# Kernel optimization log

Hardware: AMD Instinct MI355X
Metric: run time of the kernel (lower is better)

## Reference

```python
import jax, jax.numpy as jnp
from jax import lax
import numpy as np

SCALE = 3.0
TOPK = 16  # eigvec[:, -16:] in the original module
BN_EPS = 1e-5
DN = ('NCHW', 'OIHW', 'NCHW')


def setup_inputs() -> dict:
    key = jax.random.key(0)
    ks = jax.random.split(key, 8)
    B, C, H, W = 16, 256, 64, 64
    x = jax.random.normal(ks[0], (B, C, H, W), dtype=jnp.float32)
    conv1_w = jax.random.normal(ks[1], (C, C, 1, 1), dtype=jnp.float32) * (1.0 / np.sqrt(C))
    conv1_b = jax.random.normal(ks[2], (C,), dtype=jnp.float32) * 0.01
    conv2_w = jax.random.normal(ks[3], (C, C, 3, 3), dtype=jnp.float32) * (1.0 / np.sqrt(9 * C))
    bn_gamma = jnp.ones((C,), dtype=jnp.float32)
    bn_beta = jnp.zeros((C,), dtype=jnp.float32)
    bn_mean = jax.random.normal(ks[4], (C,), dtype=jnp.float32) * 0.1
    bn_var = jax.random.uniform(ks[5], (C,), dtype=jnp.float32, minval=0.5, maxval=1.5)
    return {"x": x, "conv1_w": conv1_w, "conv1_b": conv1_b, "conv2_w": conv2_w,
            "bn_gamma": bn_gamma, "bn_beta": bn_beta, "bn_mean": bn_mean, "bn_var": bn_var}


def reference(x, conv1_w, conv1_b, conv2_w, bn_gamma, bn_beta, bn_mean, bn_var):
    B, C, H, W = x.shape
    # conv1: 1x1 conv with bias
    gx = lax.conv_general_dilated(x, conv1_w, (1, 1), 'SAME', dimension_numbers=DN)
    gx = gx + conv1_b[None, :, None, None]
    # center over spatial positions: [B, C, N]
    g = gx.reshape(B, C, H * W)
    g = g - jnp.mean(g, axis=-1, keepdims=True)
    # per-batch covariance, divided by batch size (faithful to original gx.shape[0])
    cmat = jnp.einsum('bcn,bdn->bcd', g, g) / B  # [B, C, C]
    # batched symmetric eigendecomposition (ascending eigenvalues, like torch.symeig)
    _, vecs = jnp.linalg.eigh(cmat)              # vecs: [B, C, C]
    w = jnp.swapaxes(vecs[..., -TOPK:], -1, -2)  # top-16 eigvecs, [B, 16, C]
    # project onto eigvec subspace, softmax over the 16 components (dim=1)
    z = jax.nn.softmax(jnp.einsum('bkc,bcn->bkn', w, g) * SCALE, axis=1)  # [B, 16, N]
    y = jnp.einsum('bkc,bkn->bcn', w, z).reshape(B, C, H, W)
    # conv2: 3x3 conv (no bias) + BatchNorm (eval mode with running stats)
    att = lax.conv_general_dilated(y, conv2_w, (1, 1), 'SAME', dimension_numbers=DN)
    inv = bn_gamma * lax.rsqrt(bn_var + BN_EPS)
    att = att * inv[None, :, None, None] + (bn_beta - bn_mean * inv)[None, :, None, None]
    return x + att
```

## Files before the change

### kernel.cpp

```cpp
#include <hip/hip_runtime.h>
#include <hip/hip_bf16.h>
#include <math.h>


typedef __hip_bfloat16 bf16;

#define NB 16
#define NC 256
#define NSP 4096
#define LAPACK_EPS32 5.9604644775390625e-08

__device__ __forceinline__ float b2f(bf16 v){ return __bfloat162float(v); }
__device__ __forceinline__ double safelog(double x){
  double a = fabs(x);
  if (!(a > 0.0) || !isfinite(a)) a = 1e-300;
  return log(a);
}

__global__ __launch_bounds__(256) void k_detect(const unsigned short* __restrict__ xr,
                                                int* __restrict__ flags){
  __shared__ int red[256];
  int tid = threadIdx.x;
  int cnt = 0;
  for (int i = tid; i < 4096; i += 256){
    unsigned int u = xr[i];
    unsigned int e = (u >> 7) & 0xFF;
    if (e >= 134) ++cnt;
  }
  red[tid] = cnt; __syncthreads();
  for (int o=128;o>0;o>>=1){ if(tid<o) red[tid]+=red[tid+o]; __syncthreads(); }
  if (tid==0) flags[0] = (red[0] > 50) ? 1 : 0;
}

__global__ __launch_bounds__(256) void k_conv1(const void* __restrict__ xv_,
                                               const void* __restrict__ w1v,
                                               const int* __restrict__ flags,
                                               float* __restrict__ g){
  __shared__ float ws[16][256];
  int nt = blockIdx.x, ct = blockIdx.y, b = blockIdx.z;
  int tid = threadIdx.x;
  int c0 = ct*16;
  int isf = flags[0];
  if (isf){
    const float* w1 = (const float*)w1v;
    for (int i = tid; i < 16*256; i += 256)
      ws[i>>8][i&255] = w1[(size_t)(c0 + (i>>8))*256 + (i&255)];
  } else {
    const bf16* w1 = (const bf16*)w1v;
    for (int i = tid; i < 16*256; i += 256)
      ws[i>>8][i&255] = b2f(w1[(size_t)(c0 + (i>>8))*256 + (i&255)]);
  }
  __syncthreads();
  int n = nt*256 + tid;
  float acc[16];
  #pragma unroll
  for (int i=0;i<16;++i) acc[i]=0.f;
  if (isf){
    const float* xp = (const float*)xv_ + (size_t)b*NC*NSP + n;
    for (int d=0; d<256; ++d){
      float xv = xp[(size_t)d*NSP];
      #pragma unroll
      for (int i=0;i<16;++i) acc[i] = fmaf(ws[i][d], xv, acc[i]);
    }
  } else {
    const bf16* xp = (const bf16*)xv_ + (size_t)b*NC*NSP + n;
    for (int d=0; d<256; ++d){
      float xv = b2f(xp[(size_t)d*NSP]);
      #pragma unroll
      for (int i=0;i<16;++i) acc[i] = fmaf(ws[i][d], xv, acc[i]);
    }
  }
  float* gp = g + ((size_t)b*NC + c0)*NSP + n;
  #pragma unroll
  for (int i=0;i<16;++i) gp[(size_t)i*NSP] = acc[i];
}

__global__ __launch_bounds__(256) void k_center(float* __restrict__ g){
  int bc = blockIdx.x;
  float* p = g + (size_t)bc*NSP;
  int tid = threadIdx.x;
  __shared__ float red[256];
  float s = 0.f;
  for (int i=tid;i<NSP;i+=256) s += p[i];
  red[tid]=s; __syncthreads();
  for (int o=128;o>0;o>>=1){ if(tid<o) red[tid]+=red[tid+o]; __syncthreads(); }
  float mean = red[0] * (1.0f/4096.0f);
  for (int i=tid;i<NSP;i+=256) p[i] -= mean;
}

__global__ __launch_bounds__(256) void k_cmat(const float* __restrict__ g,
                                              float* __restrict__ A){
  __shared__ float t1[32][65];
  __shared__ float t2[32][65];
  int bx = blockIdx.x, by = blockIdx.y, b = blockIdx.z;
  int tid = threadIdx.x;
  int tx = tid & 31, ty = tid >> 5;
  const float* gb = g + (size_t)b*NC*NSP;
  float acc[4] = {0.f,0.f,0.f,0.f};
  for (int ch=0; ch<64; ++ch){
    int n0 = ch*64;
    for (int idx=tid; idx<2048; idx+=256){
      int r = idx>>6, cc = idx&63;
      t1[r][cc] = gb[(size_t)(by*32 + r)*NSP + n0 + cc];
      t2[r][cc] = gb[(size_t)(bx*32 + r)*NSP + n0 + cc];
    }
    __syncthreads();
    for (int kk=0; kk<64; ++kk){
      float v2 = t2[tx][kk];
      #pragma unroll
      for (int jj=0;jj<4;++jj) acc[jj] = fmaf(t1[ty+8*jj][kk], v2, acc[jj]);
    }
    __syncthreads();
  }
  #pragma unroll
  for (int jj=0;jj<4;++jj){
    int row = by*32 + ty + 8*jj, col = bx*32 + tx;
    A[((size_t)b*NC + row)*NC + col] = acc[jj]*(1.0f/16.0f);
  }
}

__global__ __launch_bounds__(256,1) void k_sytd2(float* __restrict__ Ag,
                                                 float* __restrict__ e_g,
                                                 float* __restrict__ tau_g,
                                                 float* __restrict__ d_g){
  int b = blockIdx.x, tid = threadIdx.x;
  float* A = Ag + (size_t)b*65536;
  __shared__ float v[256], wv[256], red[256];
  __shared__ float sc[2];
  for (int i=0;i<255;++i){
    float s=0.f;
    for (int r=i+2+tid; r<256; r+=256){ float a=A[(size_t)i*256+r]; s+=a*a; }
    red[tid]=s; __syncthreads();
    for(int o=128;o>0;o>>=1){ if(tid<o) red[tid]+=red[tid+o]; __syncthreads(); }
    if (tid==0){
      float xnorm2 = red[0];
      float alpha = A[(size_t)i*256+(i+1)];
      float tau=0.f, scale=0.f, beta=alpha;
      if (xnorm2 > 0.f){
        float r_ = sqrtf(alpha*alpha + xnorm2);
        beta = (alpha >= 0.f) ? -r_ : r_;
        tau = (beta - alpha)/beta;
        scale = 1.0f/(alpha - beta);
      }
      e_g[b*256+i] = beta; tau_g[b*256+i] = tau;
      sc[0]=tau; sc[1]=scale;
    }
    __syncthreads();
    float tau = sc[0], scale = sc[1];
    if (tau != 0.f){
      for (int r=i+1+tid; r<256; r+=256){
        float val = (r==i+1)?1.0f : A[(size_t)i*256+r]*scale;
        A[(size_t)i*256+r] = val;  v[r] = val;
      }
      __syncthreads();
      for (int r=i+1+tid; r<256; r+=256){
        const float* Ar = A + r;
        float acc=0.f;
        int c2 = i+1;
        for (; c2+16<=256; c2+=16){
          float av[16], vv[16];
          #pragma unroll
          for (int u=0;u<16;++u) av[u] = Ar[(size_t)(c2+u)*256];
          #pragma unroll
          for (int u=0;u<16;++u) vv[u] = v[c2+u];
          #pragma unroll
          for (int u=0;u<16;++u) acc = fmaf(av[u], vv[u], acc);
        }
        for (; c2<256; ++c2) acc = fmaf(Ar[(size_t)c2*256], v[c2], acc);
        wv[r] = tau*acc;
      }
      __syncthreads();
      float sd=0.f;
      for (int r=i+1+tid;r<256;r+=256) sd += v[r]*wv[r];
      red[tid]=sd; __syncthreads();
      for(int o=128;o>0;o>>=1){ if(tid<o) red[tid]+=red[tid+o]; __syncthreads(); }
      float a2 = -0.5f*tau*red[0];
      for (int r=i+1+tid;r<256;r+=256) wv[r] += a2*v[r];
      __syncthreads();
      int r = i+1+tid;
      if (r < 256){
        float vr=v[r], wr=wv[r];
        float* Arw = A + r;
        int c2 = i+1;
        for (; c2+16<=256; c2+=16){
          float av[16], wvv[16], vvv[16];
          #pragma unroll
          for (int u=0;u<16;++u) av[u]  = Arw[(size_t)(c2+u)*256];
          #pragma unroll
          for (int u=0;u<16;++u) wvv[u] = wv[c2+u];
          #pragma unroll
          for (int u=0;u<16;++u) vvv[u] = v[c2+u];
          #pragma unroll
          for (int u=0;u<16;++u) av[u] -= vr*wvv[u] + wr*vvv[u];
          #pragma unroll
          for (int u=0;u<16;++u) Arw[(size_t)(c2+u)*256] = av[u];
        }
        for (; c2<256; ++c2)
          Arw[(size_t)c2*256] -= vr*wv[c2] + wr*v[c2];
      }
      __syncthreads();
    }
    __syncthreads();
  }
  for (int r=tid;r<256;r+=256) d_g[b*256+r] = A[(size_t)r*256+r];
}

__global__ __launch_bounds__(256) void k_leaf(const float* __restrict__ d_g,
                                              const float* __restrict__ e_g,
                                              float* __restrict__ Qg,
                                              double* __restrict__ Dw_g,
                                              double* __restrict__ emod_g){
  int b = blockIdx.x, tid = threadIdx.x;
  float* Q = Qg + (size_t)b*65536;
  double* Dw = Dw_g + (size_t)b*256;
  __shared__ double As[16*257];
  __shared__ float  Vt[16*257];
  __shared__ double dms[256];
  __shared__ double emod[256];
  __shared__ float redf[256];

  float dv = d_g[b*256+tid];
  float ev = (tid<255)? e_g[b*256+tid] : 0.f;
  redf[tid] = fmaxf(fabsf(dv), fabsf(ev)); __syncthreads();
  for(int o=128;o>0;o>>=1){ if(tid<o) redf[tid]=fmaxf(redf[tid],redf[tid+o]); __syncthreads(); }
  double sigma = (double)redf[0];
  if (!(sigma > 0.0)) sigma = 1.0;
  double dmod = (double)dv;
  if ((tid & 15)==15 && tid<255) dmod -= fabs((double)e_g[b*256+tid]);
  if ((tid & 15)==0  && tid>0)   dmod -= fabs((double)e_g[b*256+tid-1]);
  dmod /= sigma;
  double em = (tid<255)? ((double)ev)/sigma : 0.0;
  dms[tid] = dmod;  emod[tid] = em;
  emod_g[b*256+tid] = em;
  __syncthreads();

  int l16 = tid & ~15, j = tid & 15;
  for (int r=0;r<16;++r){
    double av = 0.0;
    if (r==j)        av = dms[l16+j];
    else if (r==j-1) av = emod[l16+j-1];
    else if (r==j+1) av = emod[l16+j];
    As[r*257+tid] = av;
    Vt[r*257+tid] = (r==j)? 1.f : 0.f;
  }
  __syncthreads();

  for (int sweep=0; sweep<14; ++sweep){
    for (int p=0;p<15;++p){
      for (int q=p+1;q<16;++q){
        double app = As[p*257 + l16+p];
        double aqq = As[q*257 + l16+q];
        double apq = As[p*257 + l16+q];
        bool rot = (fabs(apq) > 1e-18);
        double c, s;
        if (rot){
          double theta = (aqq - app)/(2.0*apq);
          double t = 1.0/(fabs(theta)+sqrt(1.0+theta*theta));
          if (theta < 0.0) t = -t;
          c = 1.0/sqrt(1.0+t*t); s = t*c;
        } else { c = 1.0; s = 0.0; }
        double apj = As[p*257 + tid];
        double aqj = As[q*257 + tid];
        double npj = c*apj - s*aqj;
        double nqj = s*apj + c*aqj;
        if (rot && j==p){ npj = c*c*app - 2.0*c*s*apq + s*s*aqq; nqj = 0.0; }
        if (rot && j==q){ npj = 0.0; nqj = s*s*app + 2.0*c*s*apq + c*c*aqq; }
        As[p*257 + tid] = npj;
        As[q*257 + tid] = nqj;
        As[j*257 + l16+p] = npj;
        As[j*257 + l16+q] = nqj;
        float vp = Vt[p*257 + tid], vq = Vt[q*257 + tid];
        Vt[p*257 + tid] = (float)(c*(double)vp - s*(double)vq);
        Vt[q*257 + tid] = (float)(s*(double)vp + c*(double)vq);
      }
    }
  }
  __syncthreads();
  double myval = As[j*257 + l16+j];
  int rank = 0;
  for (int k=0;k<16;++k){
    double vk = As[k*257 + l16+k];
    if (vk < myval || (vk==myval && k<j)) ++rank;
  }
  Dw[l16+rank] = myval;
  for (int r=0;r<16;++r)
    Q[(size_t)(l16+r)*256 + (l16+rank)] = Vt[j*257 + l16+r];
}

struct DCMerge {
  double z_[256], dsv[256], ds2[256], zs2[256];
  double dl_[256], zl_[256], taus[256], ztil[256], normk[256], evo[256];
  double rotcs[256][2];
  int    cs2[256], colx[256], non_[256], defl_[256], anch[256], osrc[256], otyp[256];
  int    roti[256][2];
};

__global__ __launch_bounds__(256) void k_msolve(int lev,
                                                const double* __restrict__ emod_g,
                                                float* __restrict__ Qsrc,
                                                double* __restrict__ Dw_g,
                                                double* __restrict__ Sdl,
                                                double* __restrict__ Sztil,
                                                double* __restrict__ Staus,
                                                double* __restrict__ Snk,
                                                int* __restrict__ Scolx,
                                                int* __restrict__ Sanch,
                                                int* __restrict__ Sotyp,
                                                int* __restrict__ Sosrc,
                                                int* __restrict__ SK){
  int mrg = blockIdx.x, b = blockIdx.y, tid = threadIdx.x;
  float* Q  = Qsrc + (size_t)b*65536;
  double* Dw = Dw_g + (size_t)b*256;
  int slot = b*8 + mrg;
  __shared__ DCMerge mg;
  __shared__ int bci[4];

  int ssz = 16<<lev, nm = ssz<<1;
  int base = mrg*nm;
  double rho0 = emod_g[b*256 + base+ssz-1];
  if (tid < nm){
    float zf = (tid < ssz) ? Q[(size_t)(base+ssz-1)*256 + base + tid]
                           : Q[(size_t)(base+ssz)*256   + base + tid];
    double zz = (double)zf;
    if (rho0 < 0.0 && tid >= ssz) zz = -zz;
    mg.z_[tid] = zz * 0.70710678118654752440;
    mg.dsv[tid] = Dw[base+tid];
  }
  __syncthreads();
  double rho = fabs(2.0*rho0);
  if (tid==0){
    int i1=0, i2=ssz, o=0;
    while (i1<ssz || i2<nm){
      bool take1;
      if (i1>=ssz) take1=false; else if (i2>=nm) take1=true;
      else take1 = (mg.dsv[i1] <= mg.dsv[i2]);
      int src = take1? i1++ : i2++;
      mg.ds2[o]=mg.dsv[src]; mg.zs2[o]=mg.z_[src]; mg.cs2[o]=src; ++o;
    }
  }
  __syncthreads();
  mg.taus[tid] = (tid<nm)? fabs(mg.zs2[tid]) : 0.0; __syncthreads();
  for(int o2=128;o2>0;o2>>=1){ if(tid<o2) mg.taus[tid]=fmax(mg.taus[tid],mg.taus[tid+o2]); __syncthreads(); }
  double zmax = mg.taus[0]; __syncthreads();
  mg.taus[tid] = (tid<nm)? fabs(mg.ds2[tid]) : 0.0; __syncthreads();
  for(int o2=128;o2>0;o2>>=1){ if(tid<o2) mg.taus[tid]=fmax(mg.taus[tid],mg.taus[tid+o2]); __syncthreads(); }
  double dmax = mg.taus[0]; __syncthreads();
  double tol = 8.0*LAPACK_EPS32*fmax(dmax, zmax);
  if (tid==0){
    int K=0, nd=0, nrot=0, pj=-1;
    for (int j=0;j<nm;++j){
      if (rho*fabs(mg.zs2[j]) <= tol){ mg.defl_[nd++]=j; continue; }
      if (pj>=0){
        double sg=mg.zs2[pj], cg=mg.zs2[j];
        double tg=mg.ds2[j]-mg.ds2[pj];
        double taug=sqrt(cg*cg+sg*sg);
        double cn, sn;
        if (taug > 0.0){ cn=cg/taug; sn=-sg/taug; } else { cn=1.0; sn=0.0; }
        if (fabs(tg*cn*sn) <= tol){
          mg.zs2[j]=taug; mg.zs2[pj]=0.0;
          mg.roti[nrot][0]=mg.cs2[pj]; mg.roti[nrot][1]=mg.cs2[j];
          mg.rotcs[nrot][0]=cn; mg.rotcs[nrot][1]=sn; ++nrot;
          double t2 = mg.ds2[pj]*cn*cn + mg.ds2[j]*sn*sn;
          mg.ds2[j] = mg.ds2[pj]*sn*sn + mg.ds2[j]*cn*cn;
          mg.ds2[pj] = t2;
          mg.defl_[nd++]=pj;
          pj=j;
        } else { mg.non_[K++]=pj; pj=j; }
      } else pj=j;
    }
    if (pj>=0) mg.non_[K++]=pj;
    bci[0]=K; bci[1]=nd; bci[2]=nrot;
  }
  __syncthreads();
  int K=bci[0], nd=bci[1], nrot=bci[2];
  for (int r2=0;r2<nrot;++r2){
    int ca = base + mg.roti[r2][0], cb2 = base + mg.roti[r2][1];
    double cn = mg.rotcs[r2][0], sn = mg.rotcs[r2][1];
    if (tid < nm){
      int row = base+tid;
      float xv = Q[(size_t)row*256+ca], yv = Q[(size_t)row*256+cb2];
      Q[(size_t)row*256+ca]  = (float)(cn*(double)xv + sn*(double)yv);
      Q[(size_t)row*256+cb2] = (float)(cn*(double)yv - sn*(double)xv);
    }
    __syncthreads();
  }
  if (tid<K){
    mg.dl_[tid]=mg.ds2[mg.non_[tid]];
    mg.zl_[tid]=mg.zs2[mg.non_[tid]];
    mg.colx[tid]=mg.cs2[mg.non_[tid]];
  }
  __syncthreads();
  mg.taus[tid] = (tid<K)? mg.zl_[tid]*mg.zl_[tid] : 0.0; __syncthreads();
  for(int o2=128;o2>0;o2>>=1){ if(tid<o2) mg.taus[tid]+=mg.taus[tid+o2]; __syncthreads(); }
  double zsum2 = mg.taus[0]; __syncthreads();
  if (tid<K){
    int j=tid;
    double left=mg.dl_[j];
    double right=(j<K-1)? mg.dl_[j+1] : (mg.dl_[K-1] + rho*zsum2);
    double mid=0.5*(left+right);
    double fm=1.0;
    for (int i3=0;i3<K;++i3){
      double del=mg.dl_[i3]-mid;
      fm += rho*mg.zl_[i3]*mg.zl_[i3]/del;
    }
    int a; double lo, hi;
    if (j==K-1){
      a=K-1;
      if (fm<=0.0){ lo=mid-left; hi=right-left; } else { lo=0.0; hi=mid-left; }
    } else if (fm<=0.0){ a=j+1; lo=mid-mg.dl_[j+1]; hi=0.0; }
    else { a=j; lo=0.0; hi=mid-left; }
    double da2=mg.dl_[a];
    double t;
    if (hi > lo){
      t=0.5*(lo+hi);
    } else {
      t = (a==j)? 1e-300 : -1e-300;
      lo = fmin(lo, t); hi = fmax(hi, t);
    }
    for (int it=0; it<100; ++it){
      double gg=1.0, dg=0.0;
      for (int i3=0;i3<K;++i3){
        double del=(mg.dl_[i3]-da2)-t;
        double q=mg.zl_[i3]/del;
        gg += rho*mg.zl_[i3]*q;
        dg += rho*q*q;
      }
      if (gg<0.0) lo=t; else hi=t;
      double tn = t - gg/dg;
      if (!isfinite(tn) || !(tn>lo && tn<hi)) tn=0.5*(lo+hi);
      if (tn == 0.0) tn = (t!=0.0)? t*0.5 : ((a==j)?1e-300:-1e-300);
      double dstep=fabs(tn-t);
      t=tn;
      if (dstep <= 1e-15*(fabs(t)+1e-30)) break;
      if ((hi-lo) <= 1e-15*(fabs(da2)+fabs(t)+1e-30)) break;
    }
    if (t == 0.0 || !isfinite(t)) t = (a==j)? 1e-300 : -1e-300;
    mg.taus[j]=t; mg.anch[j]=a;
  }
  __syncthreads();
  if (tid<K){
    int i3=tid; double acc=0.0; double di=mg.dl_[i3];
    for (int j=0;j<K;++j){
      double lmd = (mg.dl_[mg.anch[j]] - di) + mg.taus[j];
      acc += safelog(lmd);
      if (j!=i3) acc -= safelog(mg.dl_[j]-di);
    }
    double mag = exp(0.5*acc);
    if (!isfinite(mag)) mag = 0.0;
    mg.ztil[i3] = (mg.zl_[i3] >= 0.0)? mag : -mag;
  }
  __syncthreads();
  if (tid<K){
    int j=tid; double da2=mg.dl_[mg.anch[j]]; double tj=mg.taus[j];
    double nr=0.0;
    for (int i3=0;i3<K;++i3){
      double del=(mg.dl_[i3]-da2)-tj;
      if (del == 0.0) del = (tj>=0.0)? -1e-300 : 1e-300;
      double sv=mg.ztil[i3]/del;
      nr += sv*sv;
    }
    if (!(nr > 0.0) || !isfinite(nr)) nr = 1.0;
    mg.normk[j]=sqrt(nr);
  }
  __syncthreads();
  if (tid==0){
    for (int a2=1;a2<nd;++a2){
      int key=mg.defl_[a2]; double kv=mg.ds2[key]; int b2=a2-1;
      while (b2>=0 && mg.ds2[mg.defl_[b2]] > kv){ mg.defl_[b2+1]=mg.defl_[b2]; --b2; }
      mg.defl_[b2+1]=key;
    }
    int i1=0,i2=0,o=0;
    while (i1<K || i2<nd){
      double v1 = (i1<K)? (mg.dl_[mg.anch[i1]]+mg.taus[i1]) : 0.0;
      double v2 = (i2<nd)? mg.ds2[mg.defl_[i2]] : 0.0;
      bool take1;
      if (i1>=K) take1=false; else if (i2>=nd) take1=true; else take1 = (v1 <= v2);
      if (take1){ mg.otyp[o]=0; mg.osrc[o]=i1; mg.evo[o]=v1; ++i1; }
      else { mg.otyp[o]=1; mg.osrc[o]=mg.cs2[mg.defl_[i2]]; mg.evo[o]=v2; ++i2; }
      ++o;
    }
  }
  __syncthreads();
  if (tid<nm) Dw[base+tid]=mg.evo[tid];
  size_t so = (size_t)slot*256;
  if (tid<K){
    Sdl[so+tid]=mg.dl_[tid]; Sztil[so+tid]=mg.ztil[tid];
    Staus[so+tid]=mg.taus[tid]; Snk[so+tid]=mg.normk[tid];
    Scolx[so+tid]=mg.colx[tid]; Sanch[so+tid]=mg.anch[tid];
  }
  if (tid<nm){ Sotyp[so+tid]=mg.otyp[tid]; Sosrc[so+tid]=mg.osrc[tid]; }
  if (tid==0) SK[slot]=K;
}

__global__ __launch_bounds__(256) void k_mvec(int lev,
                                              const float* __restrict__ Qsrc_g,
                                              float* __restrict__ Qdst_g,
                                              const double* __restrict__ Sdl,
                                              const double* __restrict__ Sztil,
                                              const double* __restrict__ Staus,
                                              const double* __restrict__ Snk,
                                              const int* __restrict__ Scolx,
                                              const int* __restrict__ Sanch,
                                              const int* __restrict__ Sotyp,
                                              const int* __restrict__ Sosrc,
                                              const int* __restrict__ SK){
  int t = blockIdx.x, mrg = blockIdx.y, b = blockIdx.z, tid = threadIdx.x;
  const float* Q = Qsrc_g + (size_t)b*65536;
  float* Qd = Qdst_g + (size_t)b*65536;
  int slot = b*8 + mrg;
  size_t so = (size_t)slot*256;
  int ssz = 16<<lev, nm = ssz<<1;
  int base = mrg*nm;
  int p0 = t*16;
  int K = SK[slot];

  __shared__ float svf[256*16];
  __shared__ double cda[16], ctj[16];
  __shared__ float cnk[16];
  __shared__ int ctyp[16], csrc[16];

  if (tid < 16){
    int p = p0 + tid;
    int typ = Sotyp[so+p], src = Sosrc[so+p];
    ctyp[tid]=typ; csrc[tid]=src;
    if (typ==0){
      int j = src;
      cda[tid] = Sdl[so + Sanch[so+j] - 0 + 0];
    }
  }
  __syncthreads();
  if (tid < 16){
    int p = p0 + tid;
    if (ctyp[tid]==0){
      int j = csrc[tid];
      int a = Sanch[so+j];
      cda[tid] = Sdl[so+a];
      ctj[tid] = Staus[so+j];
      cnk[tid] = (float)Snk[so+j];
    } else { cda[tid]=0.0; ctj[tid]=1.0; cnk[tid]=1.f; }
  }
  __syncthreads();
  for (int idx = tid; idx < K*16; idx += 256){
    int i3 = idx >> 4, c = idx & 15;
    float sv = 0.f;
    if (ctyp[c]==0){
      double del = (Sdl[so+i3] - cda[c]) - ctj[c];
      if (del == 0.0) del = (ctj[c]>=0.0)? -1e-300 : 1e-300;
      sv = (float)( Sztil[so+i3]/del / (double)cnk[c] );
      if (!isfinite(sv)) sv = 0.f;
    }
    svf[i3*16 + c] = sv;
  }
  __syncthreads();

  if (tid < nm){
    int row = base + tid;
    const float* Qr = Q + (size_t)row*256 + base;
    float acc[16];
    #pragma unroll
    for (int c=0;c<16;++c) acc[c]=0.f;
    for (int i3=0;i3<K;++i3){
      float qv = Qr[Scolx[so+i3]];
      #pragma unroll
      for (int c=0;c<16;++c) acc[c] = fmaf(qv, svf[i3*16+c], acc[c]);
    }
    #pragma unroll
    for (int c=0;c<16;++c){
      float v = acc[c];
      if (ctyp[c]==1) v = Qr[csrc[c]];
      if (!isfinite(v)) v = 0.f;
      Qd[(size_t)row*256 + base + p0 + c] = v;
    }
  }
}

__global__ __launch_bounds__(256,1) void k_backtf(const float* __restrict__ Ag,
                                                  const float* __restrict__ tau_g,
                                                  const float* __restrict__ Qg,
                                                  float* __restrict__ w16g){
  int b=blockIdx.x, tid=threadIdx.x;
  const float* A=Ag+(size_t)b*65536;
  const float* Q=Qg+(size_t)b*65536;
  __shared__ float U[256][17];
  __shared__ float pd[16][17];
  __shared__ float dk[16];
  int k=tid&15, rg=tid>>4;
  for (int r=rg;r<256;r+=16) U[r][k]=Q[(size_t)r*256+240+k];
  __syncthreads();
  for (int i=254;i>=0;--i){
    float tau=tau_g[b*256+i];
    if (tau!=0.f){
      int r0 = i+1+rg;
      float ar[16];
      #pragma unroll
      for (int u=0;u<16;++u){
        int r = r0 + u*16;
        ar[u] = (r<256)? A[(size_t)i*256+r] : 0.f;
      }
      float uv[16];
      #pragma unroll
      for (int u=0;u<16;++u){
        int r = r0 + u*16;
        uv[u] = (r<256)? U[r][k] : 0.f;
      }
      float s=0.f;
      #pragma unroll
      for (int u=0;u<16;++u){
        int r = r0 + u*16;
        if (r<256) s += ar[u]*uv[u];
      }
      pd[rg][k]=s;
      __syncthreads();
      if (tid<16){
        float acc=0.f;
        #pragma unroll
        for (int gg=0; gg<16; ++gg) acc+=pd[gg][tid];
        dk[tid]=tau*acc;
      }
      __syncthreads();
      float dkk = dk[k];
      #pragma unroll
      for (int u=0;u<16;++u){
        int r = r0 + u*16;
        if (r<256) U[r][k] -= dkk*ar[u];
      }
      __syncthreads();
    }
  }
  for (int c2=rg;c2<256;c2+=16){
    float uv = U[c2][k];
    if (!isfinite(uv)) uv = 0.f;
    w16g[((size_t)b*16+k)*256+c2]=uv;
  }
}

__global__ __launch_bounds__(256) void k_score(const float* __restrict__ g,
                                               const float* __restrict__ w16,
                                               float* __restrict__ z){
  __shared__ float ws[16][256];
  int nt=blockIdx.x, b=blockIdx.y, tid=threadIdx.x;
  for (int i=tid;i<4096;i+=256) ws[i>>8][i&255]=w16[(size_t)b*4096+i];
  __syncthreads();
  int n=nt*256+tid;
  const float* gp=g+(size_t)b*NC*NSP+n;
  float acc[16];
  #pragma unroll
  for(int k2=0;k2<16;++k2) acc[k2]=0.f;
  for (int c2=0;c2<256;++c2){
    float gv=gp[(size_t)c2*NSP];
    #pragma unroll
    for (int k2=0;k2<16;++k2) acc[k2]=fmaf(ws[k2][c2],gv,acc[k2]);
  }
  float mx=-1e30f;
  #pragma unroll
  for(int k2=0;k2<16;++k2){ acc[k2]*=3.0f; mx=fmaxf(mx,acc[k2]); }
  float sum=0.f;
  #pragma unroll
  for(int k2=0;k2<16;++k2){ acc[k2]=expf(acc[k2]-mx); sum+=acc[k2]; }
  float inv=1.0f/sum;
  float* zp=z+(size_t)b*16*NSP+n;
  #pragma unroll
  for(int k2=0;k2<16;++k2) zp[(size_t)k2*NSP]=acc[k2]*inv;
}

__global__ __launch_bounds__(256) void k_y(const float* __restrict__ z,
                                           const float* __restrict__ w16,
                                           float* __restrict__ y){
  __shared__ float ws[16][256];
  int nt=blockIdx.x, b=blockIdx.y, tid=threadIdx.x;
  for (int i=tid;i<4096;i+=256) ws[i>>8][i&255]=w16[(size_t)b*4096+i];
  __syncthreads();
  int n=nt*256+tid;
  const float* zp=z+(size_t)b*16*NSP+n;
  float zr[16];
  #pragma unroll
  for(int k2=0;k2<16;++k2) zr[k2]=zp[(size_t)k2*NSP];
  float* yp=y+(size_t)b*NC*NSP+n;
  for (int c2=0;c2<256;++c2){
    float acc=0.f;
    #pragma unroll
    for (int k2=0;k2<16;++k2) acc=fmaf(ws[k2][c2],zr[k2],acc);
    yp[(size_t)c2*NSP]=acc;
  }
}

__global__ __launch_bounds__(256) void k_conv2(const float* __restrict__ y,
                                               const void* __restrict__ w2v,
                                               const void* __restrict__ xv_,
                                               const void* __restrict__ gmv,
                                               const void* __restrict__ btv,
                                               const void* __restrict__ muv,
                                               const void* __restrict__ vrv,
                                               const int* __restrict__ flags,
                                               void* __restrict__ outv){
  __shared__ float yt[8][6][66];
  __shared__ float wt[16][8][9];
  int ht=blockIdx.x, ct=blockIdx.y, b=blockIdx.z, tid=threadIdx.x;
  int hl=tid>>6, wl=tid&63;
  int h=ht*4+hl;
  int c0=ct*16;
  int isf = flags[0];
  float acc[16];
  #pragma unroll
  for(int i=0;i<16;++i) acc[i]=0.f;
  const float* yb = y + (size_t)b*NC*NSP;
  for (int d0=0; d0<256; d0+=8){
    for (int idx=tid; idx<8*6*64; idx+=256){
      int dd=idx/384; int rem=idx-dd*384; int rr=rem>>6; int cc2=rem&63;
      int hg=ht*4-1+rr;
      float v = (hg>=0 && hg<64)? yb[(size_t)(d0+dd)*NSP + hg*64 + cc2] : 0.f;
      yt[dd][rr][cc2+1]=v;
    }
    if (tid<48){ int dd=tid/6, rr=tid-dd*6; yt[dd][rr][0]=0.f; yt[dd][rr][65]=0.f; }
    if (isf){
      const float* w2 = (const float*)w2v;
      for (int idx=tid; idx<16*8*9; idx+=256){
        int cc=idx/72; int rem=idx-cc*72; int dd=rem/9; int kk=rem-dd*9;
        wt[cc][dd][kk]=w2[ ((size_t)(c0+cc)*256 + d0+dd)*9 + kk ];
      }
    } else {
      const bf16* w2 = (const bf16*)w2v;
      for (int idx=tid; idx<16*8*9; idx+=256){
        int cc=idx/72; int rem=idx-cc*72; int dd=rem/9; int kk=rem-dd*9;
        wt[cc][dd][kk]=b2f(w2[ ((size_t)(c0+cc)*256 + d0+dd)*9 + kk ]);
      }
    }
    __syncthreads();
    for (int cc=0; cc<16; ++cc){
      float a=acc[cc];
      #pragma unroll
      for (int dd=0; dd<8; ++dd){
        const float* wp=wt[cc][dd];
        a = fmaf(wp[0], yt[dd][hl+0][wl+0], a);
        a = fmaf(wp[1], yt[dd][hl+0][wl+1], a);
        a = fmaf(wp[2], yt[dd][hl+0][wl+2], a);
        a = fmaf(wp[3], yt[dd][hl+1][wl+0], a);
        a = fmaf(wp[4], yt[dd][hl+1][wl+1], a);
        a = fmaf(wp[5], yt[dd][hl+1][wl+2], a);
        a = fmaf(wp[6], yt[dd][hl+2][wl+0], a);
        a = fmaf(wp[7], yt[dd][hl+2][wl+1], a);
        a = fmaf(wp[8], yt[dd][hl+2][wl+2], a);
      }
      acc[cc]=a;
    }
    __syncthreads();
  }
  size_t nidx=(size_t)h*64+wl;
  for (int cc=0;cc<16;++cc){
    int c=c0+cc;
    float gmf, btf, muf, vrf, xvv;
    size_t oi = ((size_t)b*NC+c)*NSP + nidx;
    if (isf){
      gmf=((const float*)gmv)[c]; btf=((const float*)btv)[c];
      muf=((const float*)muv)[c]; vrf=((const float*)vrv)[c];
      xvv=((const float*)xv_)[oi];
    } else {
      gmf=b2f(((const bf16*)gmv)[c]); btf=b2f(((const bf16*)btv)[c]);
      muf=b2f(((const bf16*)muv)[c]); vrf=b2f(((const bf16*)vrv)[c]);
      xvv=b2f(((const bf16*)xv_)[oi]);
    }
    float inv = gmf * rsqrtf(vrf + 1e-5f);
    float shift = btf - muf*inv;
    float val = xvv + acc[cc]*inv + shift;
    if (isf) ((float*)outv)[oi] = val;
    else     ((bf16*)outv)[oi] = __float2bfloat16(val);
  }
}

extern "C" void kernel_launch(void* const* d_in, const int* in_sizes, int n_in,
                              void* d_out, int out_size, void* d_ws, size_t ws_size,
                              hipStream_t stream) {
  const void* x   = d_in[0];
  const void* w1  = d_in[1];
  const void* w2  = d_in[3];
  const void* gmm = d_in[4];
  const void* bet = d_in[5];
  const void* mu  = d_in[6];
  const void* var = d_in[7];

  float* g    = (float*)d_ws;
  float* A    = g   + (size_t)NB*NC*NSP;
  float* Qa   = A   + (size_t)NB*NC*NC;
  float* Qb   = Qa  + (size_t)NB*NC*NC;
  float* w16  = Qb  + (size_t)NB*NC*NC;
  float* zb   = w16 + (size_t)NB*16*NC;
  float* e_g  = zb  + (size_t)NB*16*NSP;
  float* tau_g= e_g + (size_t)NB*NC;
  float* d_g  = tau_g + (size_t)NB*NC;
  double* Dw  = (double*)(d_g + (size_t)NB*NC);
  double* emod_g = Dw + (size_t)NB*NC;
  double* Sdl   = emod_g + (size_t)NB*NC;
  double* Sztil = Sdl   + (size_t)128*256;
  double* Staus = Sztil + (size_t)128*256;
  double* Snk   = Staus + (size_t)128*256;
  int* Scolx = (int*)(Snk + (size_t)128*256);
  int* Sanch = Scolx + (size_t)128*256;
  int* Sotyp = Sanch + (size_t)128*256;
  int* Sosrc = Sotyp + (size_t)128*256;
  int* SK    = Sosrc + (size_t)128*256;
  int* flags = SK + 256;
  size_t needed = (size_t)((char*)(flags + 16) - (char*)d_ws);
  if (ws_size < needed) return;

  hipMemsetAsync(Qa, 0, (size_t)NB*NC*NC*2*sizeof(float), stream);
  k_detect<<<dim3(1),256,0,stream>>>((const unsigned short*)x, flags);
  k_conv1 <<<dim3(16,16,16),256,0,stream>>>(x, w1, flags, g);
  k_center<<<dim3(NB*NC),256,0,stream>>>(g);
  k_cmat  <<<dim3(8,8,16),256,0,stream>>>(g, A);
  k_sytd2 <<<dim3(16),256,0,stream>>>(A, e_g, tau_g, d_g);
  k_leaf  <<<dim3(16),256,0,stream>>>(d_g, e_g, Qa, Dw, emod_g);
  k_msolve<<<dim3(8,16),256,0,stream>>>(0, emod_g, Qa, Dw, Sdl,Sztil,Staus,Snk,Scolx,Sanch,Sotyp,Sosrc,SK);
  k_mvec  <<<dim3(2,8,16),256,0,stream>>>(0, Qa, Qb, Sdl,Sztil,Staus,Snk,Scolx,Sanch,Sotyp,Sosrc,SK);
  k_msolve<<<dim3(4,16),256,0,stream>>>(1, emod_g, Qb, Dw, Sdl,Sztil,Staus,Snk,Scolx,Sanch,Sotyp,Sosrc,SK);
  k_mvec  <<<dim3(4,4,16),256,0,stream>>>(1, Qb, Qa, Sdl,Sztil,Staus,Snk,Scolx,Sanch,Sotyp,Sosrc,SK);
  k_msolve<<<dim3(2,16),256,0,stream>>>(2, emod_g, Qa, Dw, Sdl,Sztil,Staus,Snk,Scolx,Sanch,Sotyp,Sosrc,SK);
  k_mvec  <<<dim3(8,2,16),256,0,stream>>>(2, Qa, Qb, Sdl,Sztil,Staus,Snk,Scolx,Sanch,Sotyp,Sosrc,SK);
  k_msolve<<<dim3(1,16),256,0,stream>>>(3, emod_g, Qb, Dw, Sdl,Sztil,Staus,Snk,Scolx,Sanch,Sotyp,Sosrc,SK);
  k_mvec  <<<dim3(16,1,16),256,0,stream>>>(3, Qb, Qa, Sdl,Sztil,Staus,Snk,Scolx,Sanch,Sotyp,Sosrc,SK);
  k_backtf<<<dim3(16),256,0,stream>>>(A, tau_g, Qa, w16);
  k_score <<<dim3(16,16),256,0,stream>>>(g, w16, zb);
  k_y     <<<dim3(16,16),256,0,stream>>>(zb, w16, g);
  k_conv2 <<<dim3(16,16,16),256,0,stream>>>(g, w2, x, gmm, bet, mu, var, flags, d_out);
}
```

Baseline: 8.107 ms.

## Move trailing tridiagonalization submatrix into shared memory and double-buffer global loads

The Householder tridiagonalization kernel is split into two phases. The first 80 reflections still run on the global-memory matrix, now with 32-wide double-buffered loads in the symv and rank-2 update loops. The remaining 176x176 trailing block is then copied into LDS (about 124 KB) and the later steps run entirely out of shared memory. The block reduction is also replaced with a shuffle-based version, and every thread now computes tau and scale redundantly, which removes a barrier and the shared scalar broadcast. The large LDS allocation caps occupancy at one block per CU, and the 64-float register buffers add register pressure.

```diff
diff --git a/kernel.cpp b/kernel.cpp
--- a/kernel.cpp
+++ b/kernel.cpp
@@ -9,12 +9,29 @@
 #define NC 256
 #define NSP 4096
 #define LAPACK_EPS32 5.9604644775390625e-08
+
+#define PHB_I0 80
+#define PHB_M  176
 
 __device__ __forceinline__ float b2f(bf16 v){ return __bfloat162float(v); }
 __device__ __forceinline__ double safelog(double x){
   double a = fabs(x);
   if (!(a > 0.0) || !isfinite(a)) a = 1e-300;
   return log(a);
+}
+
+__device__ __forceinline__ float blk_reduce_sum(float s, float* red, int tid){
+  red[tid] = s; __syncthreads();
+  if (tid < 128) red[tid] += red[tid+128];
+  __syncthreads();
+  if (tid < 64){
+    float x = red[tid] + red[tid+64];
+    #pragma unroll
+    for (int o = 32; o > 0; o >>= 1) x += __shfl_down(x, o);
+    if (tid == 0) red[0] = x;
+  }
+  __syncthreads();
+  return red[0];
 }
 
 __global__ __launch_bounds__(256) void k_detect(const unsigned short* __restrict__ xr,
@@ -125,28 +142,22 @@
                                                  float* __restrict__ d_g){
   int b = blockIdx.x, tid = threadIdx.x;
   float* A = Ag + (size_t)b*65536;
+  __shared__ float Asub[PHB_M*PHB_M];
   __shared__ float v[256], wv[256], red[256];
-  __shared__ float sc[2];
-  for (int i=0;i<255;++i){
+
+  for (int i=0;i<PHB_I0;++i){
+    float alpha = A[(size_t)i*256+(i+1)];
     float s=0.f;
     for (int r=i+2+tid; r<256; r+=256){ float a=A[(size_t)i*256+r]; s+=a*a; }
-    red[tid]=s; __syncthreads();
-    for(int o=128;o>0;o>>=1){ if(tid<o) red[tid]+=red[tid+o]; __syncthreads(); }
-    if (tid==0){
-      float xnorm2 = red[0];
-      float alpha = A[(size_t)i*256+(i+1)];
-      float tau=0.f, scale=0.f, beta=alpha;
-      if (xnorm2 > 0.f){
-        float r_ = sqrtf(alpha*alpha + xnorm2);
-        beta = (alpha >= 0.f) ? -r_ : r_;
-        tau = (beta - alpha)/beta;
-        scale = 1.0f/(alpha - beta);
-      }
-      e_g[b*256+i] = beta; tau_g[b*256+i] = tau;
-      sc[0]=tau; sc[1]=scale;
-    }
-    __syncthreads();
-    float tau = sc[0], scale = sc[1];
+    float xnorm2 = blk_reduce_sum(s, red, tid);
+    float tau=0.f, scale=0.f, beta=alpha;
+    if (xnorm2 > 0.f){
+      float r_ = sqrtf(alpha*alpha + xnorm2);
+      beta = (alpha >= 0.f) ? -r_ : r_;
+      tau = (beta - alpha)/beta;
+      scale = 1.0f/(alpha - beta);
+    }
+    if (tid==0){ e_g[b*256+i] = beta; tau_g[b*256+i] = tau; }
     if (tau != 0.f){
       for (int r=i+1+tid; r<256; r+=256){
         float val = (r==i+1)?1.0f : A[(size_t)i*256+r]*scale;
@@ -156,53 +167,171 @@
       for (int r=i+1+tid; r<256; r+=256){
         const float* Ar = A + r;
         float acc=0.f;
-        int c2 = i+1;
-        for (; c2+16<=256; c2+=16){
-          float av[16], vv[16];
-          #pragma unroll
-          for (int u=0;u<16;++u) av[u] = Ar[(size_t)(c2+u)*256];
-          #pragma unroll
-          for (int u=0;u<16;++u) vv[u] = v[c2+u];
-          #pragma unroll
-          for (int u=0;u<16;++u) acc = fmaf(av[u], vv[u], acc);
+        int base = i+1;
+        int nfull = (256-base) >> 5;
+        float b0[32], b1[32];
+        if (nfull>0){
+          #pragma unroll
+          for (int u=0;u<32;++u) b0[u] = Ar[(size_t)(base+u)*256];
         }
-        for (; c2<256; ++c2) acc = fmaf(Ar[(size_t)c2*256], v[c2], acc);
+        int t=0;
+        for (; t+2<=nfull; t+=2){
+          int cB = base+(t+1)*32;
+          #pragma unroll
+          for (int u=0;u<32;++u) b1[u] = Ar[(size_t)(cB+u)*256];
+          int cA = base+t*32;
+          #pragma unroll
+          for (int u=0;u<32;++u) acc = fmaf(b0[u], v[cA+u], acc);
+          if (t+2 < nfull){
+            int cC = base+(t+2)*32;
+            #pragma unroll
+            for (int u=0;u<32;++u) b0[u] = Ar[(size_t)(cC+u)*256];
+          }
+          #pragma unroll
+          for (int u=0;u<32;++u) acc = fmaf(b1[u], v[cB+u], acc);
+        }
+        if (t<nfull){
+          int cA = base+t*32;
+          #pragma unroll
+          for (int u=0;u<32;++u) acc = fmaf(b0[u], v[cA+u], acc);
+          ++t;
+        }
+        for (int c2=base+nfull*32; c2<256; ++c2) acc = fmaf(Ar[(size_t)c2*256], v[c2], acc);
         wv[r] = tau*acc;
       }
       __syncthreads();
       float sd=0.f;
       for (int r=i+1+tid;r<256;r+=256) sd += v[r]*wv[r];
-      red[tid]=sd; __syncthreads();
-      for(int o=128;o>0;o>>=1){ if(tid<o) red[tid]+=red[tid+o]; __syncthreads(); }
-      float a2 = -0.5f*tau*red[0];
+      float dotv = blk_reduce_sum(sd, red, tid);
+      float a2 = -0.5f*tau*dotv;
       for (int r=i+1+tid;r<256;r+=256) wv[r] += a2*v[r];
       __syncthreads();
       int r = i+1+tid;
       if (r < 256){
         float vr=v[r], wr=wv[r];
         float* Arw = A + r;
-        int c2 = i+1;
-        for (; c2+16<=256; c2+=16){
-          float av[16], wvv[16], vvv[16];
-          #pragma unroll
-          for (int u=0;u<16;++u) av[u]  = Arw[(size_t)(c2+u)*256];
-          #pragma unroll
-          for (int u=0;u<16;++u) wvv[u] = wv[c2+u];
-          #pragma unroll
-          for (int u=0;u<16;++u) vvv[u] = v[c2+u];
-          #pragma unroll
-          for (int u=0;u<16;++u) av[u] -= vr*wvv[u] + wr*vvv[u];
-          #pragma unroll
-          for (int u=0;u<16;++u) Arw[(size_t)(c2+u)*256] = av[u];
+        int base=i+1;
+        int nfull=(256-base)>>5;
+        float b0[32], b1[32];
+        if (nfull>0){
+          #pragma unroll
+          for (int u=0;u<32;++u) b0[u] = Arw[(size_t)(base+u)*256];
         }
-        for (; c2<256; ++c2)
+        int t=0;
+        for (; t+2<=nfull; t+=2){
+          int cB = base+(t+1)*32;
+          #pragma unroll
+          for (int u=0;u<32;++u) b1[u] = Arw[(size_t)(cB+u)*256];
+          int cA = base+t*32;
+          #pragma unroll
+          for (int u=0;u<32;++u) b0[u] -= vr*wv[cA+u] + wr*v[cA+u];
+          #pragma unroll
+          for (int u=0;u<32;++u) Arw[(size_t)(cA+u)*256] = b0[u];
+          if (t+2 < nfull){
+            int cC = base+(t+2)*32;
+            #pragma unroll
+            for (int u=0;u<32;++u) b0[u] = Arw[(size_t)(cC+u)*256];
+          }
+          #pragma unroll
+          for (int u=0;u<32;++u) b1[u] -= vr*wv[cB+u] + wr*v[cB+u];
+          #pragma unroll
+          for (int u=0;u<32;++u) Arw[(size_t)(cB+u)*256] = b1[u];
+        }
+        if (t<nfull){
+          int cA = base+t*32;
+          #pragma unroll
+          for (int u=0;u<32;++u) b0[u] -= vr*wv[cA+u] + wr*v[cA+u];
+          #pragma unroll
+          for (int u=0;u<32;++u) Arw[(size_t)(cA+u)*256] = b0[u];
+          ++t;
+        }
+        for (int c2=base+nfull*32; c2<256; ++c2)
           Arw[(size_t)c2*256] -= vr*wv[c2] + wr*v[c2];
       }
       __syncthreads();
     }
     __syncthreads();
   }
-  for (int r=tid;r<256;r+=256) d_g[b*256+r] = A[(size_t)r*256+r];
+
+  for (int idx=tid; idx<PHB_M*PHB_M; idx+=256){
+    int cc = idx / PHB_M, rr = idx - cc*PHB_M;
+    Asub[idx] = A[(size_t)(PHB_I0+cc)*256 + (PHB_I0+rr)];
+  }
+  __syncthreads();
+
+  for (int i=PHB_I0;i<255;++i){
+    int cb = (i - PHB_I0)*PHB_M;
+    float alpha = Asub[cb + (i+1-PHB_I0)];
+    float s=0.f;
+    for (int r=i+2+tid; r<256; r+=256){ float a=Asub[cb + (r-PHB_I0)]; s+=a*a; }
+    float xnorm2 = blk_reduce_sum(s, red, tid);
+    float tau=0.f, scale=0.f, beta=alpha;
+    if (xnorm2 > 0.f){
+      float r_ = sqrtf(alpha*alpha + xnorm2);
+      beta = (alpha >= 0.f) ? -r_ : r_;
+      tau = (beta - alpha)/beta;
+      scale = 1.0f/(alpha - beta);
+    }
+    if (tid==0){ e_g[b*256+i] = beta; tau_g[b*256+i] = tau; }
+    if (tau != 0.f){
+      for (int r=i+1+tid; r<256; r+=256){
+        float val = (r==i+1)?1.0f : Asub[cb+(r-PHB_I0)]*scale;
+        Asub[cb+(r-PHB_I0)] = val;
+        A[(size_t)i*256+r] = val;
+        v[r] = val;
+      }
+      __syncthreads();
+      for (int r=i+1+tid; r<256; r+=256){
+        int ro = r - PHB_I0;
+        float acc=0.f;
+        int base=i+1;
+        int nfull=(256-base)>>4;
+        for (int t=0;t<nfull;++t){
+          int cA = base + t*16;
+          float av[16];
+          #pragma unroll
+          for (int u=0;u<16;++u) av[u] = Asub[(cA+u-PHB_I0)*PHB_M + ro];
+          #pragma unroll
+          for (int u=0;u<16;++u) acc = fmaf(av[u], v[cA+u], acc);
+        }
+        for (int c2=base+nfull*16;c2<256;++c2)
+          acc = fmaf(Asub[(c2-PHB_I0)*PHB_M+ro], v[c2], acc);
+        wv[r] = tau*acc;
+      }
+      __syncthreads();
+      float sd=0.f;
+      for (int r=i+1+tid;r<256;r+=256) sd += v[r]*wv[r];
+      float dotv = blk_reduce_sum(sd, red, tid);
+      float a2 = -0.5f*tau*dotv;
+      for (int r=i+1+tid;r<256;r+=256) wv[r] += a2*v[r];
+      __syncthreads();
+      int r = i+1+tid;
+      if (r < 256){
+        int ro = r - PHB_I0;
+        float vr=v[r], wr=wv[r];
+        int base=i+1;
+        int nfull=(256-base)>>4;
+        for (int t=0;t<nfull;++t){
+          int cA=base+t*16;
+          float av[16];
+          #pragma unroll
+          for (int u=0;u<16;++u) av[u] = Asub[(cA+u-PHB_I0)*PHB_M+ro];
+          #pragma unroll
+          for (int u=0;u<16;++u) av[u] -= vr*wv[cA+u] + wr*v[cA+u];
+          #pragma unroll
+          for (int u=0;u<16;++u) Asub[(cA+u-PHB_I0)*PHB_M+ro] = av[u];
+        }
+        for (int c2=base+nfull*16;c2<256;++c2)
+          Asub[(c2-PHB_I0)*PHB_M+ro] -= vr*wv[c2] + wr*v[c2];
+      }
+      __syncthreads();
+    }
+    __syncthreads();
+  }
+  for (int r=tid;r<256;r+=256){
+    float dv = (r >= PHB_I0)? Asub[(r-PHB_I0)*PHB_M + (r-PHB_I0)] : A[(size_t)r*256+r];
+    d_g[b*256+r] = dv;
+  }
 }
 
 __global__ __launch_bounds__(256) void k_leaf(const float* __restrict__ d_g,
```

After: 8.099 ms. Within noise of the previous version (-0.1%).
